# Optimization experiments

Hardware: AMD Instinct MI355X
Metric: run time of the kernel (lower is better)

## Reference

```python
import jax, jax.numpy as jnp
import numpy as np

B, T, D = 2, 1024, 2048
H = 16
NOPE, ROPE = 128, 64
QKD = NOPE + ROPE          # 192
QLORA, KVLORA = 1536, 512
VHD = 128
INTER = 8192
EPS = 1e-6
# NOTE: faithful to source: softscale = qk_head_dim * -0.5 (a large negative
# multiplier, NOT qk_head_dim ** -0.5). We reproduce the exact math.
SOFTSCALE = QKD * -0.5


def rmsnorm(x, w):
    return x * jax.lax.rsqrt(jnp.mean(jnp.square(x), axis=-1, keepdims=True) + EPS) * w


def apply_rope(x, cos, sin):
    # x: [B, T, h, rd] with rd even; cos/sin: [T, rd//2]
    x2 = x.reshape(x.shape[:-1] + (-1, 2))
    x0, x1 = x2[..., 0], x2[..., 1]
    c = cos[None, :, None, :]
    s = sin[None, :, None, :]
    r0 = x0 * c - x1 * s
    r1 = x0 * s + x1 * c
    return jnp.stack([r0, r1], axis=-1).reshape(x.shape)


def setup_inputs() -> dict:
    key = jax.random.key(0)
    ks = jax.random.split(key, 12)

    def w(k, o, i):
        return jax.random.normal(k, (o, i), jnp.float32) * 0.02

    x = jax.random.normal(ks[0], (B, T, D), jnp.float32)
    # RoPE angle tables for the rope sub-dim
    inv_freq = 1.0 / (10000.0 ** (jnp.arange(0, ROPE, 2, dtype=jnp.float32) / ROPE))
    ang = jnp.arange(T, dtype=jnp.float32)[:, None] * inv_freq[None, :]  # [T, ROPE//2]
    # causal additive mask [T, T]
    mask = jnp.where(jnp.tril(jnp.ones((T, T), bool)), 0.0, -1e9).astype(jnp.float32)
    return {
        "x": x,
        "mask": mask,
        "freqs_cos": jnp.cos(ang),
        "freqs_sin": jnp.sin(ang),
        "attn_norm_w": jnp.ones((D,), jnp.float32),
        "wq_a": w(ks[1], QLORA, D),
        "q_norm_w": jnp.ones((QLORA,), jnp.float32),
        "wq_b": w(ks[2], H * QKD, QLORA),
        "wkv_a": w(ks[3], KVLORA + ROPE, D),
        "kv_norm_w": jnp.ones((KVLORA,), jnp.float32),
        "wkv_b": w(ks[4], H * (NOPE + VHD), KVLORA),
        "wo": w(ks[5], D, H * VHD),
        "ffn_norm_w": jnp.ones((D,), jnp.float32),
        "w1": w(ks[6], INTER, D),
        "w2": w(ks[7], D, INTER),
        "w3": w(ks[8], INTER, D),
    }


def reference(x, mask, freqs_cos, freqs_sin, attn_norm_w, wq_a, q_norm_w, wq_b,
              wkv_a, kv_norm_w, wkv_b, wo, ffn_norm_w, w1, w2, w3):
    b, t, d = x.shape
    # --- MLA attention sub-block (pre-norm + residual) ---
    h = rmsnorm(x, attn_norm_w)
    # low-rank query: wq_b(q_norm(wq_a(h)))
    q = rmsnorm(h @ wq_a.T, q_norm_w) @ wq_b.T          # [b, t, H*QKD]
    q = q.reshape(b, t, H, QKD)
    q_nope, q_pe = q[..., :NOPE], q[..., NOPE:]
    q_pe = apply_rope(q_pe, freqs_cos, freqs_sin)
    # low-rank kv + decoupled rope key
    kv_all = h @ wkv_a.T                                 # [b, t, KVLORA+ROPE]
    kv_lat, k_pe = kv_all[..., :KVLORA], kv_all[..., KVLORA:]
    k_pe = apply_rope(k_pe[:, :, None, :], freqs_cos, freqs_sin)  # [b, t, 1, ROPE]
    kv = rmsnorm(kv_lat, kv_norm_w) @ wkv_b.T            # [b, t, H*(NOPE+VHD)]
    kv = kv.reshape(b, t, H, NOPE + VHD)
    k_nope, v = kv[..., :NOPE], kv[..., NOPE:]
    qf = jnp.concatenate([q_nope, q_pe], axis=-1)        # [b, t, H, QKD]
    kf = jnp.concatenate([k_nope, jnp.broadcast_to(k_pe, (b, t, H, ROPE))], axis=-1)
    scores = jnp.einsum('bshd,bthd->bsht', qf, kf) * SOFTSCALE
    scores = scores + mask[:, None, :]                   # mask over (s, 1, t)
    attn = jax.nn.softmax(scores.astype(jnp.float32), axis=-1).astype(x.dtype)
    y = jnp.einsum('bsht,bthd->bshd', attn, v).reshape(b, t, H * VHD)
    x = x + y @ wo.T
    # --- MLP sub-block (pre-norm + residual), SwiGLU ---
    h2 = rmsnorm(x, ffn_norm_w)
    out = x + (jax.nn.silu(h2 @ w1.T) * (h2 @ w3.T)) @ w2.T
    return out
```

## Files before the change

### kernel.cpp

```cpp
#include <hip/hip_runtime.h>
#include <hip/hip_bf16.h>
#include <cstddef>


#define TT 1024
#define DD 2048
#define QBLK 64
#define KVB 32

using bf16 = __hip_bfloat16;
typedef __attribute__((ext_vector_type(8))) short short8;
typedef __attribute__((ext_vector_type(8))) unsigned short ushort8v;
typedef __attribute__((ext_vector_type(4))) float f32x4;

__device__ __forceinline__ float us2f(unsigned short u) {
    return __uint_as_float(((unsigned int)u) << 16);
}
__device__ __forceinline__ float ldf(const void* p, size_t i, int isbf) {
    return isbf ? us2f(((const unsigned short*)p)[i]) : ((const float*)p)[i];
}
__device__ __forceinline__ unsigned short f2bf(float f) {
    __hip_bfloat16 b = __float2bfloat16(f);
    return *reinterpret_cast<unsigned short*>(&b);
}

__global__ __launch_bounds__(64) void detect_k(const void* __restrict__ x,
                                               int* __restrict__ flag)
{
    __shared__ int cnt;
    if (threadIdx.x == 0) cnt = 0;
    __syncthreads();
    const unsigned short* u = (const unsigned short*)x;
    int bad = 0;
    for (int i = threadIdx.x; i < 512; i += 64) {
        const float v = us2f(u[i]);
        const float a = fabsf(v);
        if (!(a < 1e6f) || (v != 0.0f && a < 1e-30f)) bad++;
    }
    atomicAdd(&cnt, bad);
    __syncthreads();
    if (threadIdx.x == 0) *flag = (cnt > 32) ? 0 : 1;
}

__global__ __launch_bounds__(256) void cvt_bf_k(
    const void* __restrict__ src, unsigned short* __restrict__ dst,
    size_t n, const int* __restrict__ flag)
{
    const int isbf = *flag;
    const size_t stride = (size_t)gridDim.x * 2048;
    for (size_t i = ((size_t)blockIdx.x * 256 + threadIdx.x) * 8; i < n; i += stride) {
        if (isbf) {
            *(ushort8v*)(dst + i) = *(const ushort8v*)((const unsigned short*)src + i);
        } else {
            const float* s = (const float*)src + i;
            float4 f0 = *(const float4*)s, f1 = *(const float4*)(s + 4);
            unsigned short t[8] = {f2bf(f0.x), f2bf(f0.y), f2bf(f0.z), f2bf(f0.w),
                                   f2bf(f1.x), f2bf(f1.y), f2bf(f1.z), f2bf(f1.w)};
            *(ushort8v*)(dst + i) = *(const ushort8v*)t;
        }
    }
}

__global__ __launch_bounds__(256) void cvt_hl_k(
    const void* __restrict__ src, unsigned short* __restrict__ dh,
    unsigned short* __restrict__ dl, size_t n, const int* __restrict__ flag)
{
    const int isbf = *flag;
    const size_t stride = (size_t)gridDim.x * 2048;
    for (size_t i = ((size_t)blockIdx.x * 256 + threadIdx.x) * 8; i < n; i += stride) {
        unsigned short th[8], tl[8];
        if (isbf) {
            const unsigned short* s = (const unsigned short*)src + i;
#pragma unroll
            for (int u = 0; u < 8; ++u) { th[u] = s[u]; tl[u] = 0; }
        } else {
            const float* s = (const float*)src + i;
#pragma unroll
            for (int u = 0; u < 8; ++u) {
                const float v = s[u];
                th[u] = f2bf(v);
                tl[u] = f2bf(v - us2f(th[u]));
            }
        }
        *(ushort8v*)(dh + i) = *(const ushort8v*)th;
        *(ushort8v*)(dl + i) = *(const ushort8v*)tl;
    }
}

template <int S, int HASR>
__global__ __launch_bounds__(256) void combine_k(
    const float* __restrict__ p, const float* __restrict__ R,
    float* __restrict__ out, int n4)
{
    const int stride = gridDim.x * 256;
    const float4* pp = (const float4*)p;
    for (int i = blockIdx.x * 256 + threadIdx.x; i < n4; i += stride) {
        float4 o = pp[i];
#pragma unroll
        for (int s = 1; s < S; ++s) {
            const float4 b4 = pp[(size_t)s * n4 + i];
            o.x += b4.x; o.y += b4.y; o.z += b4.z; o.w += b4.w;
        }
        if (HASR) {
            const float4 r4 = ((const float4*)R)[i];
            o.x += r4.x; o.y += r4.y; o.z += r4.z; o.w += r4.w;
        }
        ((float4*)out)[i] = o;
    }
}

__global__ __launch_bounds__(256) void rmsnorm_hl_k(
    const float* __restrict__ in, const void* __restrict__ w,
    unsigned short* __restrict__ oh, unsigned short* __restrict__ ol,
    int L, int istride, const int* __restrict__ flag)
{
    const int isbf = *flag;
    const int m = blockIdx.x, tid = threadIdx.x;
    const float* row = in + (size_t)m * istride;
    float ss = 0.f;
    for (int i = tid; i < L; i += 256) { float v = row[i]; ss += v * v; }
    __shared__ float red[256];
    red[tid] = ss; __syncthreads();
    for (int s = 128; s > 0; s >>= 1) {
        if (tid < s) red[tid] += red[tid + s];
        __syncthreads();
    }
    const float scale = 1.0f / sqrtf(red[0] / (float)L + 1e-6f);
    unsigned short* hrow = oh + (size_t)m * L;
    unsigned short* lrow = ol + (size_t)m * L;
    for (int i = tid; i < L; i += 256) {
        const float v = row[i] * scale * ldf(w, i, isbf);
        const unsigned short hi = f2bf(v);
        hrow[i] = hi;
        lrow[i] = f2bf(v - us2f(hi));
    }
}

__global__ __launch_bounds__(256) void rmsnorm_bf_k(
    const float* __restrict__ in, const void* __restrict__ w,
    unsigned short* __restrict__ out, int L,
    const int* __restrict__ flag)
{
    const int isbf = *flag;
    const int m = blockIdx.x, tid = threadIdx.x;
    const float* row = in + (size_t)m * L;
    float ss = 0.f;
    for (int i = tid; i < L; i += 256) { float v = row[i]; ss += v * v; }
    __shared__ float red[256];
    red[tid] = ss; __syncthreads();
    for (int s = 128; s > 0; s >>= 1) {
        if (tid < s) red[tid] += red[tid + s];
        __syncthreads();
    }
    const float scale = 1.0f / sqrtf(red[0] / (float)L + 1e-6f);
    unsigned short* orow = out + (size_t)m * L;
    for (int i = tid; i < L; i += 256)
        orow[i] = f2bf(row[i] * scale * ldf(w, i, isbf));
}

__global__ __launch_bounds__(256) void rmsnorm_x_hl_k(
    const void* __restrict__ x, size_t eoff, const void* __restrict__ w,
    unsigned short* __restrict__ hh, unsigned short* __restrict__ hl,
    float* __restrict__ xf, const int* __restrict__ flag)
{
    const int isbf = *flag;
    const int m = blockIdx.x, tid = threadIdx.x;
    const size_t base = eoff + (size_t)m * DD;
    float* xrow = xf + (size_t)m * DD;
    float ss = 0.f;
    float vals[8];
    for (int i = 0; i < 8; ++i) {
        float v = ldf(x, base + tid + 256 * i, isbf);
        vals[i] = v; ss += v * v;
        xrow[tid + 256 * i] = v;
    }
    __shared__ float red[256];
    red[tid] = ss; __syncthreads();
    for (int s = 128; s > 0; s >>= 1) {
        if (tid < s) red[tid] += red[tid + s];
        __syncthreads();
    }
    const float scale = 1.0f / sqrtf(red[0] / (float)DD + 1e-6f);
    unsigned short* hrow = hh + (size_t)m * DD;
    unsigned short* lrow = hl + (size_t)m * DD;
    for (int i = 0; i < 8; ++i) {
        const float v = vals[i] * scale * ldf(w, tid + 256 * i, isbf);
        const unsigned short hi = f2bf(v);
        hrow[tid + 256 * i] = hi;
        lrow[tid + 256 * i] = f2bf(v - us2f(hi));
    }
}

__global__ __launch_bounds__(256) void gemm_mfma3_k(
    const unsigned short* __restrict__ Ah, const unsigned short* __restrict__ Al,
    const void* __restrict__ Wv, const unsigned short* __restrict__ Wlo,
    float* __restrict__ C, int N, int K, int klen,
    int presplit, const int* __restrict__ flag)
{
    __shared__ unsigned short Ash[128 * 40];
    __shared__ unsigned short Asl[128 * 40];
    __shared__ unsigned short Wsh[128 * 40];
    __shared__ unsigned short Wsl[128 * 40];
    const int tid = threadIdx.x;
    const int lane = tid & 63;
    const int wave = tid >> 6;
    const int wm = (wave >> 1) << 6, wn = (wave & 1) << 6;
    const int bm = blockIdx.y << 7, bn = blockIdx.x << 7;
    const int k0 = blockIdx.z * klen;
    const size_t zoff = (size_t)blockIdx.z * 1024 * N;
    const int srow = tid >> 1, scol = (tid & 1) << 4;
    const unsigned short* Ahld = Ah + (size_t)(bm + srow) * K + scol;
    const unsigned short* Alld = Al + (size_t)(bm + srow) * K + scol;
    const int wrow = bn + srow;
    const size_t wldbase = (size_t)((wrow < N) ? wrow : (N - 1)) * K + scol;
    unsigned short* Ahdst = &Ash[srow * 40 + scol];
    unsigned short* Aldst = &Asl[srow * 40 + scol];
    unsigned short* Whdst = &Wsh[srow * 40 + scol];
    unsigned short* Wldst = &Wsl[srow * 40 + scol];
    const int frow = lane & 15;
    const int fk = (lane >> 4) << 3;
    const int kend = k0 + klen;

    f32x4 acc[4][4] = {};

    if (presplit) {
        const unsigned short* Whp = (const unsigned short*)Wv + wldbase;
        const unsigned short* Wlp = Wlo + wldbase;
        ushort8v ca0h = *(const ushort8v*)(Ahld + k0);
        ushort8v ca1h = *(const ushort8v*)(Ahld + k0 + 8);
        ushort8v ca0l = *(const ushort8v*)(Alld + k0);
        ushort8v ca1l = *(const ushort8v*)(Alld + k0 + 8);
        ushort8v cw0h = *(const ushort8v*)(Whp + k0);
        ushort8v cw1h = *(const ushort8v*)(Whp + k0 + 8);
        ushort8v cw0l = *(const ushort8v*)(Wlp + k0);
        ushort8v cw1l = *(const ushort8v*)(Wlp + k0 + 8);
        for (int kt = k0; kt < kend; kt += 32) {
            __syncthreads();
            *(ushort8v*)Ahdst = ca0h; *(ushort8v*)(Ahdst + 8) = ca1h;
            *(ushort8v*)Aldst = ca0l; *(ushort8v*)(Aldst + 8) = ca1l;
            *(ushort8v*)Whdst = cw0h; *(ushort8v*)(Whdst + 8) = cw1h;
            *(ushort8v*)Wldst = cw0l; *(ushort8v*)(Wldst + 8) = cw1l;
            __syncthreads();
            const int nk = (kt + 32 < kend) ? kt + 32 : kt;
            ca0h = *(const ushort8v*)(Ahld + nk);
            ca1h = *(const ushort8v*)(Ahld + nk + 8);
            ca0l = *(const ushort8v*)(Alld + nk);
            ca1l = *(const ushort8v*)(Alld + nk + 8);
            cw0h = *(const ushort8v*)(Whp + nk);
            cw1h = *(const ushort8v*)(Whp + nk + 8);
            cw0l = *(const ushort8v*)(Wlp + nk);
            cw1l = *(const ushort8v*)(Wlp + nk + 8);

            short8 afh[4], afl[4], bfh[4], bfl[4];
#pragma unroll
            for (int i = 0; i < 4; ++i) {
                afh[i] = *(const short8*)&Ash[(wm + i * 16 + frow) * 40 + fk];
                afl[i] = *(const short8*)&Asl[(wm + i * 16 + frow) * 40 + fk];
            }
#pragma unroll
            for (int j = 0; j < 4; ++j) {
                bfh[j] = *(const short8*)&Wsh[(wn + j * 16 + frow) * 40 + fk];
                bfl[j] = *(const short8*)&Wsl[(wn + j * 16 + frow) * 40 + fk];
            }
#pragma unroll
            for (int i = 0; i < 4; ++i)
#pragma unroll
                for (int j = 0; j < 4; ++j) {
                    acc[i][j] = __builtin_amdgcn_mfma_f32_16x16x32_bf16(
                        afh[i], bfh[j], acc[i][j], 0, 0, 0);
                    acc[i][j] = __builtin_amdgcn_mfma_f32_16x16x32_bf16(
                        afh[i], bfl[j], acc[i][j], 0, 0, 0);
                    acc[i][j] = __builtin_amdgcn_mfma_f32_16x16x32_bf16(
                        afl[i], bfh[j], acc[i][j], 0, 0, 0);
                }
        }
    } else {
        const int isbf = *flag;
        for (int kt = k0; kt < kend; kt += 32) {
            ushort8v a0h = *(const ushort8v*)(Ahld + kt);
            ushort8v a1h = *(const ushort8v*)(Ahld + kt + 8);
            ushort8v a0l = *(const ushort8v*)(Alld + kt);
            ushort8v a1l = *(const ushort8v*)(Alld + kt + 8);
            ushort8v w0h, w1h, w0l, w1l;
            if (isbf) {
                const unsigned short* Wp = (const unsigned short*)Wv + wldbase + kt;
                w0h = *(const ushort8v*)(Wp);
                w1h = *(const ushort8v*)(Wp + 8);
                w0l = w0h ^ w0h;
                w1l = w0l;
            } else {
                const float* Wp = (const float*)Wv + wldbase + kt;
                unsigned short th[16], tl[16];
#pragma unroll
                for (int t4 = 0; t4 < 4; ++t4) {
                    float4 f = *(const float4*)(Wp + 4 * t4);
                    float fv[4] = {f.x, f.y, f.z, f.w};
#pragma unroll
                    for (int u = 0; u < 4; ++u) {
                        const unsigned short hi = f2bf(fv[u]);
                        th[4 * t4 + u] = hi;
                        tl[4 * t4 + u] = f2bf(fv[u] - us2f(hi));
                    }
                }
                w0h = *(ushort8v*)&th[0]; w1h = *(ushort8v*)&th[8];
                w0l = *(ushort8v*)&tl[0]; w1l = *(ushort8v*)&tl[8];
            }
            __syncthreads();
            *(ushort8v*)Ahdst = a0h; *(ushort8v*)(Ahdst + 8) = a1h;
            *(ushort8v*)Aldst = a0l; *(ushort8v*)(Aldst + 8) = a1l;
            *(ushort8v*)Whdst = w0h; *(ushort8v*)(Whdst + 8) = w1h;
            *(ushort8v*)Wldst = w0l; *(ushort8v*)(Wldst + 8) = w1l;
            __syncthreads();

            short8 afh[4], afl[4], bfh[4], bfl[4];
#pragma unroll
            for (int i = 0; i < 4; ++i) {
                afh[i] = *(const short8*)&Ash[(wm + i * 16 + frow) * 40 + fk];
                afl[i] = *(const short8*)&Asl[(wm + i * 16 + frow) * 40 + fk];
            }
#pragma unroll
            for (int j = 0; j < 4; ++j) {
                bfh[j] = *(const short8*)&Wsh[(wn + j * 16 + frow) * 40 + fk];
                bfl[j] = *(const short8*)&Wsl[(wn + j * 16 + frow) * 40 + fk];
            }
#pragma unroll
            for (int i = 0; i < 4; ++i)
#pragma unroll
                for (int j = 0; j < 4; ++j) {
                    acc[i][j] = __builtin_amdgcn_mfma_f32_16x16x32_bf16(
                        afh[i], bfh[j], acc[i][j], 0, 0, 0);
                    acc[i][j] = __builtin_amdgcn_mfma_f32_16x16x32_bf16(
                        afh[i], bfl[j], acc[i][j], 0, 0, 0);
                    acc[i][j] = __builtin_amdgcn_mfma_f32_16x16x32_bf16(
                        afl[i], bfh[j], acc[i][j], 0, 0, 0);
                }
        }
    }

#pragma unroll
    for (int i = 0; i < 4; ++i) {
        const int r0 = bm + wm + i * 16 + ((lane >> 4) << 2);
#pragma unroll
        for (int j = 0; j < 4; ++j) {
            const int c = bn + wn + j * 16 + (lane & 15);
            if (c < N) {
#pragma unroll
                for (int g = 0; g < 4; ++g)
                    C[zoff + (size_t)(r0 + g) * N + c] = acc[i][j][g];
            }
        }
    }
}

template <int EPI>
__global__ __launch_bounds__(256) void gemm_mfma_k(
    const unsigned short* __restrict__ A, const void* __restrict__ Wv,
    const float* __restrict__ R, void* __restrict__ outp,
    int N, int K, int klen, int wready, const int* __restrict__ flag)
{
    __shared__ unsigned short As[128 * 40];
    __shared__ unsigned short Ws[128 * 40];
    const int tid = threadIdx.x;
    const int lane = tid & 63;
    const int wave = tid >> 6;
    const int wm = (wave >> 1) << 6, wn = (wave & 1) << 6;
    const int bm = blockIdx.y << 7, bn = blockIdx.x << 7;
    const int k0 = blockIdx.z * klen;
    const size_t zoff = (size_t)blockIdx.z * 1024 * N;
    const int srow = tid >> 1, scol = (tid & 1) << 4;
    const unsigned short* Ald = A + (size_t)(bm + srow) * K + scol;
    const size_t wldbase = (size_t)(bn + srow) * K + scol;
    unsigned short* Adst = &As[srow * 40 + scol];
    unsigned short* Wdst = &Ws[srow * 40 + scol];
    const int frow = lane & 15;
    const int fk = (lane >> 4) << 3;
    const int kend = k0 + klen;

    f32x4 acc[4][4] = {};

    if (wready) {
        const unsigned short* Wp = (const unsigned short*)Wv + wldbase;
        ushort8v ca0 = *(const ushort8v*)(Ald + k0);
        ushort8v ca1 = *(const ushort8v*)(Ald + k0 + 8);
        ushort8v cw0 = *(const ushort8v*)(Wp + k0);
        ushort8v cw1 = *(const ushort8v*)(Wp + k0 + 8);
        for (int kt = k0; kt < kend; kt += 32) {
            __syncthreads();
            *(ushort8v*)Adst = ca0; *(ushort8v*)(Adst + 8) = ca1;
            *(ushort8v*)Wdst = cw0; *(ushort8v*)(Wdst + 8) = cw1;
            __syncthreads();
            const int nk = (kt + 32 < kend) ? kt + 32 : kt;
            ca0 = *(const ushort8v*)(Ald + nk);
            ca1 = *(const ushort8v*)(Ald + nk + 8);
            cw0 = *(const ushort8v*)(Wp + nk);
            cw1 = *(const ushort8v*)(Wp + nk + 8);

            short8 af[4], bfr[4];
#pragma unroll
            for (int i = 0; i < 4; ++i)
                af[i] = *(const short8*)&As[(wm + i * 16 + frow) * 40 + fk];
#pragma unroll
            for (int j = 0; j < 4; ++j)
                bfr[j] = *(const short8*)&Ws[(wn + j * 16 + frow) * 40 + fk];
#pragma unroll
            for (int i = 0; i < 4; ++i)
#pragma unroll
                for (int j = 0; j < 4; ++j)
                    acc[i][j] = __builtin_amdgcn_mfma_f32_16x16x32_bf16(
                        af[i], bfr[j], acc[i][j], 0, 0, 0);
        }
    } else {
        const int isbf = *flag;
        for (int kt = k0; kt < kend; kt += 32) {
            ushort8v a0 = *(const ushort8v*)(Ald + kt);
            ushort8v a1 = *(const ushort8v*)(Ald + kt + 8);
            ushort8v w0, w1;
            if (isbf) {
                const unsigned short* Wp = (const unsigned short*)Wv + wldbase + kt;
                w0 = *(const ushort8v*)(Wp);
                w1 = *(const ushort8v*)(Wp + 8);
            } else {
                const float* Wp = (const float*)Wv + wldbase + kt;
                float4 f0 = *(const float4*)(Wp);
                float4 f1 = *(const float4*)(Wp + 4);
                float4 f2 = *(const float4*)(Wp + 8);
                float4 f3 = *(const float4*)(Wp + 12);
                unsigned short wt[16];
                wt[0] = f2bf(f0.x); wt[1] = f2bf(f0.y); wt[2]  = f2bf(f0.z); wt[3]  = f2bf(f0.w);
                wt[4] = f2bf(f1.x); wt[5] = f2bf(f1.y); wt[6]  = f2bf(f1.z); wt[7]  = f2bf(f1.w);
                wt[8] = f2bf(f2.x); wt[9] = f2bf(f2.y); wt[10] = f2bf(f2.z); wt[11] = f2bf(f2.w);
                wt[12] = f2bf(f3.x); wt[13] = f2bf(f3.y); wt[14] = f2bf(f3.z); wt[15] = f2bf(f3.w);
                w0 = *(const ushort8v*)&wt[0];
                w1 = *(const ushort8v*)&wt[8];
            }
            __syncthreads();
            *(ushort8v*)Adst = a0; *(ushort8v*)(Adst + 8) = a1;
            *(ushort8v*)Wdst = w0; *(ushort8v*)(Wdst + 8) = w1;
            __syncthreads();

            short8 af[4], bfr[4];
#pragma unroll
            for (int i = 0; i < 4; ++i)
                af[i] = *(const short8*)&As[(wm + i * 16 + frow) * 40 + fk];
#pragma unroll
            for (int j = 0; j < 4; ++j)
                bfr[j] = *(const short8*)&Ws[(wn + j * 16 + frow) * 40 + fk];
#pragma unroll
            for (int i = 0; i < 4; ++i)
#pragma unroll
                for (int j = 0; j < 4; ++j)
                    acc[i][j] = __builtin_amdgcn_mfma_f32_16x16x32_bf16(
                        af[i], bfr[j], acc[i][j], 0, 0, 0);
        }
    }

#pragma unroll
    for (int i = 0; i < 4; ++i) {
        const int r0 = bm + wm + i * 16 + ((lane >> 4) << 2);
#pragma unroll
        for (int j = 0; j < 4; ++j) {
            const int c = bn + wn + j * 16 + (lane & 15);
#pragma unroll
            for (int g = 0; g < 4; ++g) {
                const size_t idx = zoff + (size_t)(r0 + g) * N + c;
                const float v = acc[i][j][g];
                if (EPI == 0) {
                    ((float*)outp)[idx] = v;
                } else if (EPI == 1) {
                    ((float*)outp)[idx] = v + R[idx];
                } else {
                    const float gv = R[idx];
                    const float sg = 1.0f / (1.0f + __expf(-gv));
                    ((unsigned short*)outp)[idx] = f2bf(gv * sg * v);
                }
            }
        }
    }
}

__global__ __launch_bounds__(256) void rope_k(
    float* __restrict__ qb, float* __restrict__ kva,
    const void* __restrict__ fc, const void* __restrict__ fs,
    const int* __restrict__ flag)
{
    const int isbf = *flag;
    const int t = blockIdx.x;
    const int tid = threadIdx.x;
    __shared__ float c[32], s[32];
    if (tid < 32) {
        c[tid] = ldf(fc, t * 32 + tid, isbf);
        s[tid] = ldf(fs, t * 32 + tid, isbf);
    }
    __syncthreads();
    for (int p = tid; p < 512; p += 256) {
        const int h = p >> 5, i = p & 31;
        float* base = qb + (size_t)t * 3072 + h * 192 + 128 + 2 * i;
        const float x0 = base[0], x1 = base[1];
        base[0] = x0 * c[i] - x1 * s[i];
        base[1] = x0 * s[i] + x1 * c[i];
    }
    if (tid < 32) {
        float* base = kva + (size_t)t * 576 + 512 + 2 * tid;
        const float x0 = base[0], x1 = base[1];
        base[0] = x0 * c[tid] - x1 * s[tid];
        base[1] = x0 * s[tid] + x1 * c[tid];
    }
}

__global__ __launch_bounds__(256) void kvprep_k(
    const float* __restrict__ kvb,
    const float* __restrict__ kva,
    unsigned short* __restrict__ kh, unsigned short* __restrict__ kl,
    unsigned short* __restrict__ vt)
{
    const int tt = blockIdx.x, h = blockIdx.y;
    const int tid = threadIdx.x;
    const int tbase = tt * 64;
    for (int i = tid; i < 64 * 192; i += 256) {
        const int t = i / 192, k = i % 192;
        const float v = (k < 128)
            ? kvb[(size_t)(tbase + t) * 4096 + h * 256 + k]
            : kva[(size_t)(tbase + t) * 576 + 512 + (k - 128)];
        const unsigned short hi = f2bf(v);
        const size_t o = ((size_t)h * 1024 + tbase + t) * 192 + k;
        kh[o] = hi;
        kl[o] = f2bf(v - us2f(hi));
    }
    __shared__ unsigned short Vl[128][72];
    for (int i = tid; i < 64 * 128; i += 256) {
        const int t = i >> 7, d = i & 127;
        Vl[d][t] = f2bf(kvb[(size_t)(tbase + t) * 4096 + h * 256 + 128 + d]);
    }
    __syncthreads();
    for (int i = tid; i < 128 * 64; i += 256) {
        const int d = i >> 6, t = i & 63;
        vt[((size_t)h * 128 + d) * 1024 + tbase + t] = Vl[d][t];
    }
}

__global__ __launch_bounds__(256) void attn_mfma_k(
    const float* __restrict__ qb,
    const unsigned short* __restrict__ kh,
    const unsigned short* __restrict__ kl,
    const unsigned short* __restrict__ vt,
    unsigned short* __restrict__ y)
{
    const int qt = blockIdx.x, h = blockIdx.y;
    const int s0 = qt * QBLK;
    const int tid = threadIdx.x;
    const int lane = tid & 63, wave = tid >> 6;
    const int frow = lane & 15;
    const int fk8 = (lane >> 4) << 3;
    const int g4 = (lane >> 4) << 2;

    __shared__ __align__(16) unsigned short Ksh[KVB][200];
    __shared__ __align__(16) unsigned short Ksl[KVB][200];
    __shared__ __align__(16) unsigned short Vs[128][40];
    __shared__ __align__(16) unsigned short Ps[4][16][40];

    const int wrow0 = s0 + wave * 16;
    short8 qhf[6], qlf[6];
    {
        const float* qrow = qb + (size_t)(wrow0 + frow) * 3072 + h * 192 + fk8;
#pragma unroll
        for (int ks = 0; ks < 6; ++ks) {
            float4 f0 = *(const float4*)(qrow + ks * 32);
            float4 f1 = *(const float4*)(qrow + ks * 32 + 4);
            float fv[8] = {f0.x, f0.y, f0.z, f0.w, f1.x, f1.y, f1.z, f1.w};
            unsigned short th[8], tl[8];
#pragma unroll
            for (int u = 0; u < 8; ++u) {
                th[u] = f2bf(fv[u]);
                tl[u] = f2bf(fv[u] - us2f(th[u]));
            }
            qhf[ks] = *(short8*)th;
            qlf[ks] = *(short8*)tl;
        }
    }

    f32x4 O[8] = {};
    float m_run[4] = {-1e30f, -1e30f, -1e30f, -1e30f};
    float l_run[4] = {};

    const int ntiles = (s0 + QBLK) / KVB;
    for (int tt = 0; tt < ntiles; ++tt) {
        const int t0 = tt * KVB;
        __syncthreads();
        for (int i = tid; i < KVB * 24; i += 256) {
            const int r = i / 24, c = (i % 24) * 8;
            const size_t gof = ((size_t)h * 1024 + t0 + r) * 192 + c;
            *(ushort8v*)&Ksh[r][c] = *(const ushort8v*)(kh + gof);
            *(ushort8v*)&Ksl[r][c] = *(const ushort8v*)(kl + gof);
        }
        for (int i = tid; i < 128 * 4; i += 256) {
            const int d = i >> 2, c = (i & 3) * 8;
            *(ushort8v*)&Vs[d][c] =
                *(const ushort8v*)(vt + ((size_t)h * 128 + d) * 1024 + t0 + c);
        }
        __syncthreads();

        const bool active = (t0 <= wrow0 + 15);
        if (active) {
            f32x4 s[2] = {};
#pragma unroll
            for (int j = 0; j < 2; ++j) {
                const unsigned short* kb = &Ksh[j * 16 + frow][fk8];
                const unsigned short* lb = &Ksl[j * 16 + frow][fk8];
#pragma unroll
                for (int ks = 0; ks < 6; ++ks) {
                    short8 bh = *(const short8*)(kb + ks * 32);
                    short8 bl = *(const short8*)(lb + ks * 32);
                    s[j] = __builtin_amdgcn_mfma_f32_16x16x32_bf16(qhf[ks], bh, s[j], 0, 0, 0);
                    s[j] = __builtin_amdgcn_mfma_f32_16x16x32_bf16(qhf[ks], bl, s[j], 0, 0, 0);
                    s[j] = __builtin_amdgcn_mfma_f32_16x16x32_bf16(qlf[ks], bh, s[j], 0, 0, 0);
                }
            }
            const bool edge = (t0 + KVB - 1 > wrow0);
            float sv[2][4];
#pragma unroll
            for (int j = 0; j < 2; ++j)
#pragma unroll
                for (int g = 0; g < 4; ++g) {
                    float v = s[j][g] * -96.0f;
                    if (edge) {
                        const int col = t0 + j * 16 + frow;
                        const int row = wrow0 + g4 + g;
                        if (col > row) v = -1e30f;
                    }
                    sv[j][g] = v;
                }
            float alpha[4];
#pragma unroll
            for (int g = 0; g < 4; ++g) {
                float mt = fmaxf(sv[0][g], sv[1][g]);
                mt = fmaxf(mt, __shfl_xor(mt, 1));
                mt = fmaxf(mt, __shfl_xor(mt, 2));
                mt = fmaxf(mt, __shfl_xor(mt, 4));
                mt = fmaxf(mt, __shfl_xor(mt, 8));
                const float mn = fmaxf(m_run[g], mt);
                alpha[g] = __expf(m_run[g] - mn);
                m_run[g] = mn;
                const float p0 = __expf(sv[0][g] - mn);
                const float p1 = __expf(sv[1][g] - mn);
                sv[0][g] = p0; sv[1][g] = p1;
                float ps = p0 + p1;
                ps += __shfl_xor(ps, 1);
                ps += __shfl_xor(ps, 2);
                ps += __shfl_xor(ps, 4);
                ps += __shfl_xor(ps, 8);
                l_run[g] = l_run[g] * alpha[g] + ps;
            }
#pragma unroll
            for (int jt = 0; jt < 8; ++jt)
#pragma unroll
                for (int g = 0; g < 4; ++g)
                    O[jt][g] *= alpha[g];
#pragma unroll
            for (int j = 0; j < 2; ++j)
#pragma unroll
                for (int g = 0; g < 4; ++g)
                    Ps[wave][g4 + g][j * 16 + frow] = f2bf(sv[j][g]);
        }
        __syncthreads();
        if (active) {
            short8 pa = *(const short8*)&Ps[wave][frow][fk8];
#pragma unroll
            for (int jt = 0; jt < 8; ++jt) {
                short8 vb = *(const short8*)&Vs[jt * 16 + frow][fk8];
                O[jt] = __builtin_amdgcn_mfma_f32_16x16x32_bf16(pa, vb, O[jt], 0, 0, 0);
            }
        }
    }

#pragma unroll
    for (int g = 0; g < 4; ++g) {
        const float invl = 1.0f / l_run[g];
        const int row = wrow0 + g4 + g;
        unsigned short* yo = y + (size_t)row * 2048 + h * 128;
#pragma unroll
        for (int jt = 0; jt < 8; ++jt)
            yo[jt * 16 + frow] = f2bf(O[jt][g] * invl);
    }
}

extern "C" void kernel_launch(void* const* d_in, const int* in_sizes, int n_in,
                              void* d_out, int out_size, void* d_ws, size_t ws_size,
                              hipStream_t stream) {
    (void)in_sizes; (void)n_in; (void)out_size;
    const void* x       = d_in[0];
    const void* fcos    = d_in[2];
    const void* fsin    = d_in[3];
    const void* attn_nw = d_in[4];
    const void* wq_a    = d_in[5];
    const void* q_nw    = d_in[6];
    const void* wq_b    = d_in[7];
    const void* wkv_a   = d_in[8];
    const void* kv_nw   = d_in[9];
    const void* wkv_b   = d_in[10];
    const void* wo      = d_in[11];
    const void* ffn_nw  = d_in[12];
    const void* w1      = d_in[13];
    const void* w2      = d_in[14];
    const void* w3      = d_in[15];

    int* flag = (int*)d_ws;
    float* a  = (float*)d_ws + 64;
    const size_t M1 = 1048576;
    float* xf  = a;
    unsigned short* hh = (unsigned short*)(a + 2 * M1);
    unsigned short* hl = (unsigned short*)(a + 3 * M1);
    float* qa  = a + 4 * M1;
    float* kva = a + 4 * M1;
    unsigned short* kvnh = (unsigned short*)(a + 4 * M1 + 655360);
    unsigned short* kvnl = (unsigned short*)(a + 4 * M1 + 655360 + 262144);
    unsigned short* qah = (unsigned short*)(a + 5 * M1 + 524288);
    unsigned short* qal = (unsigned short*)(a + 6 * M1 + 262144);
    float* qb  = a + 7 * M1;
    float* kvb = a + 10 * M1;
    unsigned short* kh = (unsigned short*)(a + 2 * M1);
    unsigned short* kl = (unsigned short*)(a + 5 * M1 + 524288);
    unsigned short* vt = (unsigned short*)(a + 14 * M1);
    unsigned short* yb = (unsigned short*)(a + 3 * M1 + 524288);
    unsigned short* hb  = (unsigned short*)(a + 2 * M1);
    float* gb  = a + 4 * M1;
    unsigned short* gb2 = (unsigned short*)(a + 12 * M1);
    float* x2  = xf;
    float* sp  = a + 10 * M1;
    float* fpo = a + 5 * M1;
    float* fp2 = a + 2 * M1;
    unsigned short* wo_b  = (unsigned short*)(a + 16 * M1);
    unsigned short* w1_b  = (unsigned short*)(a + 18 * M1);
    unsigned short* w3_b  = (unsigned short*)(a + 26 * M1);
    unsigned short* w2_b  = (unsigned short*)(a + 34 * M1);
    unsigned short* wqa_h = (unsigned short*)(a + 42 * M1);
    unsigned short* wqa_l = wqa_h + 3145728u;
    unsigned short* wqb_h = (unsigned short*)(a + 45 * M1);
    unsigned short* wqb_l = wqb_h + 4718592u;
    unsigned short* wkva_h = (unsigned short*)(a + 49 * M1 + 524288);
    unsigned short* wkva_l = wkva_h + 1179648u;
    unsigned short* wkvb_h = (unsigned short*)(a + 50 * M1 + 655360);
    unsigned short* wkvb_l = wkvb_h + 2097152u;
    const size_t NEED = 256 + (size_t)(52 * M1 + 655360) * 4;
    const int prep = (ws_size >= NEED) ? 1 : 0;

    detect_k<<<1, 64, 0, stream>>>(x, flag);

    if (prep) {
        cvt_bf_k<<<1024, 256, 0, stream>>>(wo, wo_b, (size_t)2048 * 2048, flag);
        cvt_bf_k<<<2048, 256, 0, stream>>>(w1, w1_b, (size_t)8192 * 2048, flag);
        cvt_bf_k<<<2048, 256, 0, stream>>>(w3, w3_b, (size_t)8192 * 2048, flag);
        cvt_bf_k<<<2048, 256, 0, stream>>>(w2, w2_b, (size_t)2048 * 8192, flag);
        cvt_hl_k<<<1024, 256, 0, stream>>>(wq_a, wqa_h, wqa_l, (size_t)1536 * 2048, flag);
        cvt_hl_k<<<1024, 256, 0, stream>>>(wq_b, wqb_h, wqb_l, (size_t)3072 * 1536, flag);
        cvt_hl_k<<<512, 256, 0, stream>>>(wkv_a, wkva_h, wkva_l, (size_t)576 * 2048, flag);
        cvt_hl_k<<<1024, 256, 0, stream>>>(wkv_b, wkvb_h, wkvb_l, (size_t)4096 * 512, flag);
    }
    const void* Wqa = prep ? (const void*)wqa_h : wq_a;
    const void* Wqb = prep ? (const void*)wqb_h : wq_b;
    const void* Wkva = prep ? (const void*)wkva_h : wkv_a;
    const void* Wkvb = prep ? (const void*)wkvb_h : wkv_b;
    const unsigned short* WqaL = prep ? wqa_l : nullptr;
    const unsigned short* WqbL = prep ? wqb_l : nullptr;
    const unsigned short* WkvaL = prep ? wkva_l : nullptr;
    const unsigned short* WkvbL = prep ? wkvb_l : nullptr;
    const void* WoP = prep ? (const void*)wo_b : wo;
    const void* W1P = prep ? (const void*)w1_b : w1;
    const void* W3P = prep ? (const void*)w3_b : w3;
    const void* W2P = prep ? (const void*)w2_b : w2;

    for (int b = 0; b < 2; ++b) {
        const size_t eoff = (size_t)b * TT * DD;
        float* outb = (float*)d_out + eoff;

        rmsnorm_x_hl_k<<<TT, 256, 0, stream>>>(x, eoff, attn_nw, hh, hl, xf, flag);
        gemm_mfma3_k<<<dim3(12, 8, 4), 256, 0, stream>>>(hh, hl, Wqa, WqaL, sp, 1536, 2048, 512, prep, flag);
        combine_k<4, 0><<<1024, 256, 0, stream>>>(sp, nullptr, qa, 393216);
        rmsnorm_hl_k<<<TT, 256, 0, stream>>>(qa, q_nw, qah, qal, 1536, 1536, flag);
        gemm_mfma3_k<<<dim3(24, 8, 2), 256, 0, stream>>>(qah, qal, Wqb, WqbL, sp, 3072, 1536, 768, prep, flag);
        combine_k<2, 0><<<1024, 256, 0, stream>>>(sp, nullptr, qb, 786432);
        gemm_mfma3_k<<<dim3(5, 8, 8), 256, 0, stream>>>(hh, hl, Wkva, WkvaL, sp, 576, 2048, 256, prep, flag);
        combine_k<8, 0><<<1024, 256, 0, stream>>>(sp, nullptr, kva, 147456);
        rmsnorm_hl_k<<<TT, 256, 0, stream>>>(kva, kv_nw, kvnh, kvnl, 512, 576, flag);
        rope_k<<<TT, 256, 0, stream>>>(qb, kva, fcos, fsin, flag);
        gemm_mfma3_k<<<dim3(32, 8, 1), 256, 0, stream>>>(kvnh, kvnl, Wkvb, WkvbL, kvb, 4096, 512, 512, prep, flag);
        kvprep_k<<<dim3(16, 16), 256, 0, stream>>>(kvb, kva, kh, kl, vt);
        attn_mfma_k<<<dim3(TT / QBLK, 16), 256, 0, stream>>>(qb, kh, kl, vt, yb);

        gemm_mfma_k<0><<<dim3(16, 8, 4), 256, 0, stream>>>(yb, WoP, nullptr, fpo, 2048, 2048, 512, prep, flag);
        combine_k<4, 1><<<1024, 256, 0, stream>>>(fpo, xf, x2, 524288);
        rmsnorm_bf_k<<<TT, 256, 0, stream>>>(x2, ffn_nw, hb, 2048, flag);
        gemm_mfma_k<0><<<dim3(64, 8, 1), 256, 0, stream>>>(hb, W1P, nullptr, gb, 8192, 2048, 2048, prep, flag);
        gemm_mfma_k<3><<<dim3(64, 8, 1), 256, 0, stream>>>(hb, W3P, gb, gb2, 8192, 2048, 2048, prep, flag);
        gemm_mfma_k<0><<<dim3(16, 8, 4), 256, 0, stream>>>(gb2, W2P, nullptr, fp2, 2048, 8192, 2048, prep, flag);
        combine_k<4, 1><<<1024, 256, 0, stream>>>(fp2, x2, outb, 524288);
    }
}
```

Before: 1.351 ms.

## Fuse W1/W3 SwiGLU GEMMs and split attention KV range with merge kernel

Replaces the separate W1 and W3 GEMMs with one kernel that computes both accumulators from a shared A tile and applies SiLU gating in the epilogue. This avoids writing and re-reading the fp32 gate buffer. Attention is split into two KV halves per query block along grid z, which doubles parallelism. Each half writes its partial output together with its running max and sum, and a new merge kernel combines them. The fused GEMM doubles accumulator register use, and the partial outputs are stored in bf16, which adds a small rounding step.

New measurement: 1.345 ms. No clear change (-0.5%).

```diff
diff --git a/kernel.cpp b/kernel.cpp
--- a/kernel.cpp
+++ b/kernel.cpp
@@ -478,6 +478,146 @@
     }
 }
 
+__global__ __launch_bounds__(256) void gemm_swiglu_k(
+    const unsigned short* __restrict__ A, const void* __restrict__ W1v,
+    const void* __restrict__ W3v, unsigned short* __restrict__ outp,
+    int N, int K, int wready, const int* __restrict__ flag)
+{
+    __shared__ unsigned short As[128 * 40];
+    __shared__ unsigned short Ws1[128 * 40];
+    __shared__ unsigned short Ws3[128 * 40];
+    const int tid = threadIdx.x;
+    const int lane = tid & 63;
+    const int wave = tid >> 6;
+    const int wm = (wave >> 1) << 6, wn = (wave & 1) << 6;
+    const int bm = blockIdx.y << 7, bn = blockIdx.x << 7;
+    const int srow = tid >> 1, scol = (tid & 1) << 4;
+    const unsigned short* Ald = A + (size_t)(bm + srow) * K + scol;
+    const size_t wldbase = (size_t)(bn + srow) * K + scol;
+    unsigned short* Adst = &As[srow * 40 + scol];
+    unsigned short* W1dst = &Ws1[srow * 40 + scol];
+    unsigned short* W3dst = &Ws3[srow * 40 + scol];
+    const int frow = lane & 15;
+    const int fk = (lane >> 4) << 3;
+
+    f32x4 acc1[4][4] = {};
+    f32x4 acc3[4][4] = {};
+
+    if (wready) {
+        const unsigned short* W1p = (const unsigned short*)W1v + wldbase;
+        const unsigned short* W3p = (const unsigned short*)W3v + wldbase;
+        ushort8v ca0 = *(const ushort8v*)(Ald);
+        ushort8v ca1 = *(const ushort8v*)(Ald + 8);
+        ushort8v c10 = *(const ushort8v*)(W1p);
+        ushort8v c11 = *(const ushort8v*)(W1p + 8);
+        ushort8v c30 = *(const ushort8v*)(W3p);
+        ushort8v c31 = *(const ushort8v*)(W3p + 8);
+        for (int kt = 0; kt < K; kt += 32) {
+            __syncthreads();
+            *(ushort8v*)Adst = ca0; *(ushort8v*)(Adst + 8) = ca1;
+            *(ushort8v*)W1dst = c10; *(ushort8v*)(W1dst + 8) = c11;
+            *(ushort8v*)W3dst = c30; *(ushort8v*)(W3dst + 8) = c31;
+            __syncthreads();
+            const int nk = (kt + 32 < K) ? kt + 32 : kt;
+            ca0 = *(const ushort8v*)(Ald + nk);
+            ca1 = *(const ushort8v*)(Ald + nk + 8);
+            c10 = *(const ushort8v*)(W1p + nk);
+            c11 = *(const ushort8v*)(W1p + nk + 8);
+            c30 = *(const ushort8v*)(W3p + nk);
+            c31 = *(const ushort8v*)(W3p + nk + 8);
+
+            short8 af[4], b1[4], b3[4];
+#pragma unroll
+            for (int i = 0; i < 4; ++i)
+                af[i] = *(const short8*)&As[(wm + i * 16 + frow) * 40 + fk];
+#pragma unroll
+            for (int j = 0; j < 4; ++j) {
+                b1[j] = *(const short8*)&Ws1[(wn + j * 16 + frow) * 40 + fk];
+                b3[j] = *(const short8*)&Ws3[(wn + j * 16 + frow) * 40 + fk];
+            }
+#pragma unroll
+            for (int i = 0; i < 4; ++i)
+#pragma unroll
+                for (int j = 0; j < 4; ++j) {
+                    acc1[i][j] = __builtin_amdgcn_mfma_f32_16x16x32_bf16(
+                        af[i], b1[j], acc1[i][j], 0, 0, 0);
+                    acc3[i][j] = __builtin_amdgcn_mfma_f32_16x16x32_bf16(
+                        af[i], b3[j], acc3[i][j], 0, 0, 0);
+                }
+        }
+    } else {
+        const int isbf = *flag;
+        for (int kt = 0; kt < K; kt += 32) {
+            ushort8v a0 = *(const ushort8v*)(Ald + kt);
+            ushort8v a1 = *(const ushort8v*)(Ald + kt + 8);
+            ushort8v w10, w11, w30, w31;
+            if (isbf) {
+                const unsigned short* W1p = (const unsigned short*)W1v + wldbase + kt;
+                const unsigned short* W3p = (const unsigned short*)W3v + wldbase + kt;
+                w10 = *(const ushort8v*)(W1p); w11 = *(const ushort8v*)(W1p + 8);
+                w30 = *(const ushort8v*)(W3p); w31 = *(const ushort8v*)(W3p + 8);
+            } else {
+                const float* W1p = (const float*)W1v + wldbase + kt;
+                const float* W3p = (const float*)W3v + wldbase + kt;
+                unsigned short t1[16], t3[16];
+#pragma unroll
+                for (int t4 = 0; t4 < 4; ++t4) {
+                    float4 f1 = *(const float4*)(W1p + 4 * t4);
+                    float4 f3 = *(const float4*)(W3p + 4 * t4);
+                    float v1[4] = {f1.x, f1.y, f1.z, f1.w};
+                    float v3[4] = {f3.x, f3.y, f3.z, f3.w};
+#pragma unroll
+                    for (int u = 0; u < 4; ++u) {
+                        t1[4 * t4 + u] = f2bf(v1[u]);
+                        t3[4 * t4 + u] = f2bf(v3[u]);
+                    }
+                }
+                w10 = *(ushort8v*)&t1[0]; w11 = *(ushort8v*)&t1[8];
+                w30 = *(ushort8v*)&t3[0]; w31 = *(ushort8v*)&t3[8];
+            }
+            __syncthreads();
+            *(ushort8v*)Adst = a0; *(ushort8v*)(Adst + 8) = a1;
+            *(ushort8v*)W1dst = w10; *(ushort8v*)(W1dst + 8) = w11;
+            *(ushort8v*)W3dst = w30; *(ushort8v*)(W3dst + 8) = w31;
+            __syncthreads();
+
+            short8 af[4], b1[4], b3[4];
+#pragma unroll
+            for (int i = 0; i < 4; ++i)
+                af[i] = *(const short8*)&As[(wm + i * 16 + frow) * 40 + fk];
+#pragma unroll
+            for (int j = 0; j < 4; ++j) {
+                b1[j] = *(const short8*)&Ws1[(wn + j * 16 + frow) * 40 + fk];
+                b3[j] = *(const short8*)&Ws3[(wn + j * 16 + frow) * 40 + fk];
+            }
+#pragma unroll
+            for (int i = 0; i < 4; ++i)
+#pragma unroll
+                for (int j = 0; j < 4; ++j) {
+                    acc1[i][j] = __builtin_amdgcn_mfma_f32_16x16x32_bf16(
+                        af[i], b1[j], acc1[i][j], 0, 0, 0);
+                    acc3[i][j] = __builtin_amdgcn_mfma_f32_16x16x32_bf16(
+                        af[i], b3[j], acc3[i][j], 0, 0, 0);
+                }
+        }
+    }
+
+#pragma unroll
+    for (int i = 0; i < 4; ++i) {
+        const int r0 = bm + wm + i * 16 + ((lane >> 4) << 2);
+#pragma unroll
+        for (int j = 0; j < 4; ++j) {
+            const int c = bn + wn + j * 16 + (lane & 15);
+#pragma unroll
+            for (int g = 0; g < 4; ++g) {
+                const float gv = acc1[i][j][g];
+                const float sg = 1.0f / (1.0f + __expf(-gv));
+                outp[(size_t)(r0 + g) * N + c] = f2bf(gv * sg * acc3[i][j][g]);
+            }
+        }
+    }
+}
+
 __global__ __launch_bounds__(256) void rope_k(
     float* __restrict__ qb, float* __restrict__ kva,
     const void* __restrict__ fc, const void* __restrict__ fs,
@@ -543,9 +683,9 @@
     const unsigned short* __restrict__ kh,
     const unsigned short* __restrict__ kl,
     const unsigned short* __restrict__ vt,
-    unsigned short* __restrict__ y)
-{
-    const int qt = blockIdx.x, h = blockIdx.y;
+    float* __restrict__ opart)
+{
+    const int qt = blockIdx.x, h = blockIdx.y, z = blockIdx.z;
     const int s0 = qt * QBLK;
     const int tid = threadIdx.x;
     const int lane = tid & 63, wave = tid >> 6;
@@ -582,8 +722,9 @@
     float m_run[4] = {-1e30f, -1e30f, -1e30f, -1e30f};
     float l_run[4] = {};
 
-    const int ntiles = (s0 + QBLK) / KVB;
-    for (int tt = 0; tt < ntiles; ++tt) {
+    const int t_beg = z * (qt + 1);
+    const int t_end = t_beg + (qt + 1);
+    for (int tt = t_beg; tt < t_end; ++tt) {
         const int t0 = tt * KVB;
         __syncthreads();
         for (int i = tid; i < KVB * 24; i += 256) {
@@ -674,12 +815,32 @@
 
 #pragma unroll
     for (int g = 0; g < 4; ++g) {
-        const float invl = 1.0f / l_run[g];
         const int row = wrow0 + g4 + g;
-        unsigned short* yo = y + (size_t)row * 2048 + h * 128;
+        float* rec = opart + (((size_t)z * 1024 + row) * 16 + h) * 66;
+        unsigned short* ob = (unsigned short*)rec;
 #pragma unroll
         for (int jt = 0; jt < 8; ++jt)
-            yo[jt * 16 + frow] = f2bf(O[jt][g] * invl);
+            ob[jt * 16 + frow] = f2bf(O[jt][g]);
+        if ((lane & 15) == 0) { rec[64] = m_run[g]; rec[65] = l_run[g]; }
+    }
+}
+
+__global__ __launch_bounds__(256) void attn_merge_k(
+    const float* __restrict__ opart, unsigned short* __restrict__ y)
+{
+    const int r = blockIdx.x;
+    for (int i = threadIdx.x; i < 2048; i += 256) {
+        const int h = i >> 7, d = i & 127;
+        const float* r0 = opart + (((size_t)r) * 16 + h) * 66;
+        const float* r1 = opart + (((size_t)1024 + r) * 16 + h) * 66;
+        const float m0 = r0[64], l0 = r0[65];
+        const float m1 = r1[64], l1 = r1[65];
+        const float mm = fmaxf(m0, m1);
+        const float a0 = __expf(m0 - mm), a1 = __expf(m1 - mm);
+        const float denom = l0 * a0 + l1 * a1;
+        const float o0 = us2f(((const unsigned short*)r0)[d]);
+        const float o1 = us2f(((const unsigned short*)r1)[d]);
+        y[(size_t)r * 2048 + h * 128 + d] = f2bf((o0 * a0 + o1 * a1) / denom);
     }
 }
 
@@ -722,12 +883,12 @@
     unsigned short* vt = (unsigned short*)(a + 14 * M1);
     unsigned short* yb = (unsigned short*)(a + 3 * M1 + 524288);
     unsigned short* hb  = (unsigned short*)(a + 2 * M1);
-    float* gb  = a + 4 * M1;
     unsigned short* gb2 = (unsigned short*)(a + 12 * M1);
     float* x2  = xf;
     float* sp  = a + 10 * M1;
     float* fpo = a + 5 * M1;
     float* fp2 = a + 2 * M1;
+    float* opart = a + 10 * M1;
     unsigned short* wo_b  = (unsigned short*)(a + 16 * M1);
     unsigned short* w1_b  = (unsigned short*)(a + 18 * M1);
     unsigned short* w3_b  = (unsigned short*)(a + 26 * M1);
@@ -784,13 +945,13 @@
         rope_k<<<TT, 256, 0, stream>>>(qb, kva, fcos, fsin, flag);
         gemm_mfma3_k<<<dim3(32, 8, 1), 256, 0, stream>>>(kvnh, kvnl, Wkvb, WkvbL, kvb, 4096, 512, 512, prep, flag);
         kvprep_k<<<dim3(16, 16), 256, 0, stream>>>(kvb, kva, kh, kl, vt);
-        attn_mfma_k<<<dim3(TT / QBLK, 16), 256, 0, stream>>>(qb, kh, kl, vt, yb);
+        attn_mfma_k<<<dim3(TT / QBLK, 16, 2), 256, 0, stream>>>(qb, kh, kl, vt, opart);
+        attn_merge_k<<<TT, 256, 0, stream>>>(opart, yb);
 
         gemm_mfma_k<0><<<dim3(16, 8, 4), 256, 0, stream>>>(yb, WoP, nullptr, fpo, 2048, 2048, 512, prep, flag);
         combine_k<4, 1><<<1024, 256, 0, stream>>>(fpo, xf, x2, 524288);
         rmsnorm_bf_k<<<TT, 256, 0, stream>>>(x2, ffn_nw, hb, 2048, flag);
-        gemm_mfma_k<0><<<dim3(64, 8, 1), 256, 0, stream>>>(hb, W1P, nullptr, gb, 8192, 2048, 2048, prep, flag);
-        gemm_mfma_k<3><<<dim3(64, 8, 1), 256, 0, stream>>>(hb, W3P, gb, gb2, 8192, 2048, 2048, prep, flag);
+        gemm_swiglu_k<<<dim3(64, 8), 256, 0, stream>>>(hb, W1P, W3P, gb2, 8192, 2048, prep, flag);
         gemm_mfma_k<0><<<dim3(16, 8, 4), 256, 0, stream>>>(gb2, W2P, nullptr, fp2, 2048, 8192, 2048, prep, flag);
         combine_k<4, 1><<<1024, 256, 0, stream>>>(fp2, x2, outb, 524288);
     }
```
